# Kernel optimization log

Measured on AMD Instinct MI355X. Metric: run time of the kernel, lower is better.

Reference implementation:

```python
import jax, jax.numpy as jnp
import numpy as np

N_NODES = 24
BATCH = 65536

def _build_edge_index():
    # hard-coded 24-node supply-chain DAG from the source: node i (i<22, even pair)
    # connects to nodes 2*(i//2)+2 and 2*(i//2)+3
    rows, cols = [], []
    for i in range(22):
        base = 2 * (i // 2) + 2
        rows += [i, i]
        cols += [base, base + 1]
    return jnp.asarray(np.stack([rows, cols]), dtype=jnp.int64)  # [2, 44]


def setup_inputs() -> dict:
    key = jax.random.key(0)
    ks = jax.random.split(key, 4)
    x = jax.random.normal(ks[0], (BATCH, N_NODES, 10), dtype=jnp.float32)
    W1 = jax.random.normal(ks[1], (10, 64), dtype=jnp.float32) * (1.0 / np.sqrt(10))
    b1 = jnp.zeros((64,), dtype=jnp.float32)
    W3 = jax.random.normal(ks[2], (64, 64), dtype=jnp.float32) * (1.0 / 8.0)
    b3 = jnp.zeros((64,), dtype=jnp.float32)
    W2 = jax.random.normal(ks[3], (64, 10), dtype=jnp.float32) * (1.0 / 8.0)
    b2 = jnp.zeros((10,), dtype=jnp.float32)
    edge_index = _build_edge_index()
    return {"x": x, "W1": W1, "b1": b1, "W3": W3, "b3": b3,
            "W2": W2, "b2": b2, "edge_index": edge_index}


def _gcn_norm(edge_index, n_nodes):
    # PyG gcn_norm with add_self_loops=True: deg counted at target (col) index
    src, dst = edge_index[0], edge_index[1]
    deg = jnp.ones((n_nodes,), jnp.float32).at[dst].add(1.0)  # self loop contributes 1
    dinv = jax.lax.rsqrt(deg)
    norm_e = dinv[src] * dinv[dst]        # [E] edge weights
    norm_self = dinv * dinv               # [N] self-loop weights
    return src, dst, norm_e, norm_self


def _gcn_conv(h, W, b, src, dst, norm_e, norm_self):
    # h: [B, N, Fin] -> [B, N, Fout]
    hw = h @ W                                             # [B, N, Fout]
    msg = hw[:, src, :] * norm_e[None, :, None]            # gather + scale [B, E, Fout]
    agg = jnp.zeros_like(hw).at[:, dst, :].add(msg)        # scatter-add over targets
    agg = agg + hw * norm_self[None, :, None]              # self loops
    return agg + b


def reference(x, W1, b1, W3, b3, W2, b2, edge_index):
    src, dst, norm_e, norm_self = _gcn_norm(edge_index, x.shape[1])
    h = jax.nn.relu(_gcn_conv(x, W1, b1, src, dst, norm_e, norm_self))
    h = jax.nn.relu(_gcn_conv(h, W3, b3, src, dst, norm_e, norm_self))
    msg = jax.nn.relu(_gcn_conv(h, W2, b2, src, dst, norm_e, norm_self))  # [B, N, 10]
    pool = jnp.mean(msg, axis=1)  # global_mean_pool over the 24 nodes -> [B, 10]
    return pool
```

## Files before the change

### kernel.cpp

```cpp
#include <hip/hip_runtime.h>
#include <hip/hip_bf16.h>


typedef __attribute__((ext_vector_type(8))) short bf16x8;
typedef __attribute__((ext_vector_type(4))) float f32x4;

#define NBLK  1024
#define ITERS 8

__device__ __forceinline__ unsigned short f2bf(float f) {
  __hip_bfloat16 h = __float2bfloat16(f);
  return __builtin_bit_cast(unsigned short, h);
}
__device__ __forceinline__ float bflo(unsigned d) {
  return __builtin_bit_cast(float, d << 16);
}
__device__ __forceinline__ float bfhi(unsigned d) {
  return __builtin_bit_cast(float, d & 0xffff0000u);
}

union U16 { uint4 u; bf16x8 b; };

__device__ __forceinline__ bf16x8 pack8(const float v[8]) {
  U16 un;
  un.u.x = (unsigned)f2bf(v[0]) | ((unsigned)f2bf(v[1]) << 16);
  un.u.y = (unsigned)f2bf(v[2]) | ((unsigned)f2bf(v[3]) << 16);
  un.u.z = (unsigned)f2bf(v[4]) | ((unsigned)f2bf(v[5]) << 16);
  un.u.w = (unsigned)f2bf(v[6]) | ((unsigned)f2bf(v[7]) << 16);
  return un.b;
}

__global__ __launch_bounds__(256, 2)
void gnn_kernel(const float* __restrict__ xg,  const float* __restrict__ w1g,
                const float* __restrict__ b1g, const float* __restrict__ w3g,
                const float* __restrict__ b3g, const float* __restrict__ w2g,
                const float* __restrict__ b2g, float* __restrict__ outg) {
  __shared__ unsigned short hbuf_s[4][48 * 72];
  __shared__ float          o3_s[4][48 * 20];

  const int tid  = threadIdx.x;
  const int w    = tid >> 6;
  const int lane = tid & 63;
  const int l15  = lane & 15;
  const int g    = lane >> 4;
  unsigned short* hb = hbuf_s[w];
  float*          o3 = o3_s[w];
  const int wgid = blockIdx.x * 4 + w;

  bf16x8 w1f[4], w3f[4][2], w2f[2];
  {
    float v[8];
    #pragma unroll
    for (int mi = 0; mi < 4; ++mi) {
      const int c = 16 * mi + l15;
      #pragma unroll
      for (int j = 0; j < 8; ++j) { int k = 8 * g + j; v[j] = (k < 10) ? w1g[k * 64 + c] : 0.f; }
      w1f[mi] = pack8(v);
      #pragma unroll
      for (int ki = 0; ki < 2; ++ki) {
        #pragma unroll
        for (int j = 0; j < 8; ++j) { int k = 32 * ki + 8 * g + j; v[j] = w3g[k * 64 + c]; }
        w3f[mi][ki] = pack8(v);
      }
    }
    #pragma unroll
    for (int ki = 0; ki < 2; ++ki) {
      #pragma unroll
      for (int j = 0; j < 8; ++j) {
        int k = 32 * ki + 8 * g + j;
        v[j] = (l15 < 10) ? w2g[k * 10 + l15] : 0.f;
      }
      w2f[ki] = pack8(v);
    }
  }

  float b1r[2][8], b3r[2][8];
  #pragma unroll
  for (int ki = 0; ki < 2; ++ki) {
    float4 t0 = *(const float4*)&b1g[32 * ki + 8 * g];
    float4 t1 = *(const float4*)&b1g[32 * ki + 8 * g + 4];
    b1r[ki][0] = t0.x; b1r[ki][1] = t0.y; b1r[ki][2] = t0.z; b1r[ki][3] = t0.w;
    b1r[ki][4] = t1.x; b1r[ki][5] = t1.y; b1r[ki][6] = t1.z; b1r[ki][7] = t1.w;
    float4 s0v = *(const float4*)&b3g[32 * ki + 8 * g];
    float4 s1v = *(const float4*)&b3g[32 * ki + 8 * g + 4];
    b3r[ki][0] = s0v.x; b3r[ki][1] = s0v.y; b3r[ki][2] = s0v.z; b3r[ki][3] = s0v.w;
    b3r[ki][4] = s1v.x; b3r[ki][5] = s1v.y; b3r[ki][6] = s1v.z; b3r[ki][7] = s1v.w;
  }
  const float b2p = b2g[lane % 10];

  int rowA[3], rowB[3], xoff[3];
  float csv[3], cabv[3];
  #pragma unroll
  for (int ni = 0; ni < 3; ++ni) {
    const int r   = 16 * ni + l15;
    const int sub = r / 24;
    const int n   = r - 24 * sub;
    csv[ni]  = (n < 2) ? 1.f : (1.f / 3.f);
    cabv[ni] = (n < 2) ? 0.f : ((n < 4) ? 0.57735026918962576f : (1.f / 3.f));
    const int sA = (n < 4) ? 0 : ((n & ~1) - 2);
    const int sB = (n < 4) ? 1 : ((n & ~1) - 1);
    rowA[ni] = 24 * sub + sA;
    rowB[ni] = 24 * sub + sB;
    xoff[ni] = sub * 240 + n * 10;
  }

  auto build = [&](int ni, int ki, const float(&bias)[8]) -> bf16x8 {
    const int kbase = 32 * ki + 8 * g;
    const int rS = 16 * ni + l15;
    const uint4 vS = *(const uint4*)(hb + rS * 72 + kbase);
    const uint4 vA = *(const uint4*)(hb + rowA[ni] * 72 + kbase);
    const uint4 vB = *(const uint4*)(hb + rowB[ni] * 72 + kbase);
    const float cs = csv[ni], cab = cabv[ni];
    const unsigned aS[4] = {vS.x, vS.y, vS.z, vS.w};
    const unsigned aA[4] = {vA.x, vA.y, vA.z, vA.w};
    const unsigned aB[4] = {vB.x, vB.y, vB.z, vB.w};
    unsigned d[4];
    #pragma unroll
    for (int p = 0; p < 4; ++p) {
      float lo = fmaxf(cs * bflo(aS[p]) + cab * (bflo(aA[p]) + bflo(aB[p])) + bias[2 * p],     0.f);
      float hi = fmaxf(cs * bfhi(aS[p]) + cab * (bfhi(aA[p]) + bfhi(aB[p])) + bias[2 * p + 1], 0.f);
      d[p] = (unsigned)f2bf(lo) | ((unsigned)f2bf(hi) << 16);
    }
    U16 un; un.u.x = d[0]; un.u.y = d[1]; un.u.z = d[2]; un.u.w = d[3];
    return un.b;
  };

  const f32x4 zf = {0.f, 0.f, 0.f, 0.f};

  for (int it = 0; it < ITERS; ++it) {
    const int s0 = wgid * (2 * ITERS) + it * 2;
    const float* xb = xg + (long)s0 * 240;

    f32x4 acc[4][3];
    #pragma unroll
    for (int ni = 0; ni < 3; ++ni) {
      float v[8] = {0.f, 0.f, 0.f, 0.f, 0.f, 0.f, 0.f, 0.f};
      const float* xr = xb + xoff[ni];
      if (g == 0) {
        float2 p0 = *(const float2*)(xr + 0);
        float2 p1 = *(const float2*)(xr + 2);
        float2 p2 = *(const float2*)(xr + 4);
        float2 p3 = *(const float2*)(xr + 6);
        v[0] = p0.x; v[1] = p0.y; v[2] = p1.x; v[3] = p1.y;
        v[4] = p2.x; v[5] = p2.y; v[6] = p3.x; v[7] = p3.y;
      } else if (g == 1) {
        float2 p4 = *(const float2*)(xr + 8);
        v[0] = p4.x; v[1] = p4.y;
      }
      bf16x8 bx = pack8(v);
      #pragma unroll
      for (int mi = 0; mi < 4; ++mi)
        acc[mi][ni] = __builtin_amdgcn_mfma_f32_16x16x32_bf16(w1f[mi], bx, zf, 0, 0, 0);
    }
    #pragma unroll
    for (int mi = 0; mi < 4; ++mi) {
      #pragma unroll
      for (int ni = 0; ni < 3; ++ni) {
        const int r = 16 * ni + l15, cb = 16 * mi + 4 * g;
        uint2 pk;
        pk.x = (unsigned)f2bf(acc[mi][ni][0]) | ((unsigned)f2bf(acc[mi][ni][1]) << 16);
        pk.y = (unsigned)f2bf(acc[mi][ni][2]) | ((unsigned)f2bf(acc[mi][ni][3]) << 16);
        *(uint2*)(hb + r * 72 + cb) = pk;
      }
    }
    __syncthreads();

    #pragma unroll
    for (int ni = 0; ni < 3; ++ni) {
      bf16x8 bb0 = build(ni, 0, b1r[0]);
      bf16x8 bb1 = build(ni, 1, b1r[1]);
      #pragma unroll
      for (int mi = 0; mi < 4; ++mi) {
        f32x4 t = __builtin_amdgcn_mfma_f32_16x16x32_bf16(w3f[mi][0], bb0, zf, 0, 0, 0);
        acc[mi][ni] = __builtin_amdgcn_mfma_f32_16x16x32_bf16(w3f[mi][1], bb1, t, 0, 0, 0);
      }
    }
    #pragma unroll
    for (int mi = 0; mi < 4; ++mi) {
      #pragma unroll
      for (int ni = 0; ni < 3; ++ni) {
        const int r = 16 * ni + l15, cb = 16 * mi + 4 * g;
        uint2 pk;
        pk.x = (unsigned)f2bf(acc[mi][ni][0]) | ((unsigned)f2bf(acc[mi][ni][1]) << 16);
        pk.y = (unsigned)f2bf(acc[mi][ni][2]) | ((unsigned)f2bf(acc[mi][ni][3]) << 16);
        *(uint2*)(hb + r * 72 + cb) = pk;
      }
    }
    __syncthreads();

    f32x4 acc3[3];
    #pragma unroll
    for (int ni = 0; ni < 3; ++ni) {
      bf16x8 bb0 = build(ni, 0, b3r[0]);
      bf16x8 bb1 = build(ni, 1, b3r[1]);
      f32x4 t  = __builtin_amdgcn_mfma_f32_16x16x32_bf16(w2f[0], bb0, zf, 0, 0, 0);
      acc3[ni] = __builtin_amdgcn_mfma_f32_16x16x32_bf16(w2f[1], bb1, t, 0, 0, 0);
    }
    #pragma unroll
    for (int ni = 0; ni < 3; ++ni) {
      const int r = 16 * ni + l15;
      *(f32x4*)(o3 + r * 20 + 4 * g) = acc3[ni];
    }
    __syncthreads();

    {
      const int part = lane / 10;
      const int pc   = lane - 10 * part;
      #pragma unroll
      for (int sub = 0; sub < 2; ++sub) {
        float sum = 0.f;
        if (lane < 60) {
          const int rb = 24 * sub;
          #pragma unroll
          for (int dn = 0; dn < 4; ++dn) {
            const int n = 4 * part + dn;
            const float cs  = (n < 2) ? 1.f : (1.f / 3.f);
            const float cab = (n < 2) ? 0.f : ((n < 4) ? 0.57735026918962576f : (1.f / 3.f));
            const int sA = (n < 4) ? 0 : ((n & ~1) - 2);
            const int sB = (n < 4) ? 1 : ((n & ~1) - 1);
            const float vv = cs * o3[(rb + n) * 20 + pc]
                           + cab * (o3[(rb + sA) * 20 + pc] + o3[(rb + sB) * 20 + pc]);
            sum += fmaxf(vv + b2p, 0.f);
          }
        }
        float s1 = sum + __shfl_down(sum, 30);
        float t1 = __shfl_down(s1, 10);
        float t2 = __shfl_down(s1, 20);
        float tot = s1 + t1 + t2;
        if (lane < 10) outg[(long)(s0 + sub) * 10 + lane] = tot * (1.f / 24.f);
      }
    }
    __syncthreads();
  }
}

extern "C" void kernel_launch(void* const* d_in, const int* in_sizes, int n_in,
                              void* d_out, int out_size, void* d_ws, size_t ws_size,
                              hipStream_t stream) {
  (void)in_sizes; (void)n_in; (void)d_ws; (void)ws_size; (void)out_size;
  const float* x  = (const float*)d_in[0];
  const float* W1 = (const float*)d_in[1];
  const float* b1 = (const float*)d_in[2];
  const float* W3 = (const float*)d_in[3];
  const float* b3 = (const float*)d_in[4];
  const float* W2 = (const float*)d_in[5];
  const float* b2 = (const float*)d_in[6];
  float* out = (float*)d_out;
  hipLaunchKernelGGL(gnn_kernel, dim3(NBLK), dim3(256), 0, stream,
                     x, W1, b1, W3, b3, W2, b2, out);
}
```

Baseline: 209.7 us.

## Drop block barriers, alias LDS buffers, raise occupancy, use packed fp32 math

Removes every block-wide __syncthreads from the per-iteration loop. Each wave only touches its own private LDS slice, so in-wave LDS ordering is relied on instead of barriers. The layer-3 output buffer now shares storage with the hidden-state buffer, which cuts LDS per block, and launch bounds go from 2 to 4 blocks per CU. The aggregate-plus-ReLU step is rewritten with two-wide float vectors and elementwise fma/max so the compiler can emit packed fp32 instructions. The risk is that correctness now rests on wave-local LDS ordering and on the buffer aliasing, and the tighter register budget could cause spills.

```diff
diff --git a/kernel.cpp b/kernel.cpp
--- a/kernel.cpp
+++ b/kernel.cpp
@@ -4,6 +4,7 @@
 
 typedef __attribute__((ext_vector_type(8))) short bf16x8;
 typedef __attribute__((ext_vector_type(4))) float f32x4;
+typedef __attribute__((ext_vector_type(2))) float f32x2;
 
 #define NBLK  1024
 #define ITERS 8
@@ -12,11 +13,14 @@
   __hip_bfloat16 h = __float2bfloat16(f);
   return __builtin_bit_cast(unsigned short, h);
 }
-__device__ __forceinline__ float bflo(unsigned d) {
-  return __builtin_bit_cast(float, d << 16);
-}
-__device__ __forceinline__ float bfhi(unsigned d) {
-  return __builtin_bit_cast(float, d & 0xffff0000u);
+__device__ __forceinline__ f32x2 unpk(unsigned d) {
+  f32x2 r;
+  r.x = __builtin_bit_cast(float, d << 16);
+  r.y = __builtin_bit_cast(float, d & 0xffff0000u);
+  return r;
+}
+__device__ __forceinline__ unsigned pack2(f32x2 v) {
+  return (unsigned)f2bf(v.x) | ((unsigned)f2bf(v.y) << 16);
 }
 
 union U16 { uint4 u; bf16x8 b; };
@@ -30,13 +34,12 @@
   return un.b;
 }
 
-__global__ __launch_bounds__(256, 2)
+__global__ __launch_bounds__(256, 4)
 void gnn_kernel(const float* __restrict__ xg,  const float* __restrict__ w1g,
                 const float* __restrict__ b1g, const float* __restrict__ w3g,
                 const float* __restrict__ b3g, const float* __restrict__ w2g,
                 const float* __restrict__ b2g, float* __restrict__ outg) {
-  __shared__ unsigned short hbuf_s[4][48 * 72];
-  __shared__ float          o3_s[4][48 * 20];
+  __shared__ __align__(16) unsigned short hbuf_s[4][48 * 72];
 
   const int tid  = threadIdx.x;
   const int w    = tid >> 6;
@@ -44,7 +47,7 @@
   const int l15  = lane & 15;
   const int g    = lane >> 4;
   unsigned short* hb = hbuf_s[w];
-  float*          o3 = o3_s[w];
+  float*          o3 = (float*)hbuf_s[w];
   const int wgid = blockIdx.x * 4 + w;
 
   bf16x8 w1f[4], w3f[4][2], w2f[2];
@@ -74,17 +77,15 @@
     }
   }
 
-  float b1r[2][8], b3r[2][8];
+  f32x2 b1r[2][4], b3r[2][4];
   #pragma unroll
   for (int ki = 0; ki < 2; ++ki) {
-    float4 t0 = *(const float4*)&b1g[32 * ki + 8 * g];
-    float4 t1 = *(const float4*)&b1g[32 * ki + 8 * g + 4];
-    b1r[ki][0] = t0.x; b1r[ki][1] = t0.y; b1r[ki][2] = t0.z; b1r[ki][3] = t0.w;
-    b1r[ki][4] = t1.x; b1r[ki][5] = t1.y; b1r[ki][6] = t1.z; b1r[ki][7] = t1.w;
-    float4 s0v = *(const float4*)&b3g[32 * ki + 8 * g];
-    float4 s1v = *(const float4*)&b3g[32 * ki + 8 * g + 4];
-    b3r[ki][0] = s0v.x; b3r[ki][1] = s0v.y; b3r[ki][2] = s0v.z; b3r[ki][3] = s0v.w;
-    b3r[ki][4] = s1v.x; b3r[ki][5] = s1v.y; b3r[ki][6] = s1v.z; b3r[ki][7] = s1v.w;
+    #pragma unroll
+    for (int p = 0; p < 4; ++p) {
+      const int k = 32 * ki + 8 * g + 2 * p;
+      b1r[ki][p].x = b1g[k]; b1r[ki][p].y = b1g[k + 1];
+      b3r[ki][p].x = b3g[k]; b3r[ki][p].y = b3g[k + 1];
+    }
   }
   const float b2p = b2g[lane % 10];
 
@@ -104,22 +105,27 @@
     xoff[ni] = sub * 240 + n * 10;
   }
 
-  auto build = [&](int ni, int ki, const float(&bias)[8]) -> bf16x8 {
+  const f32x2 zero2 = {0.f, 0.f};
+
+  auto build = [&](int ni, int ki, const f32x2(&bias)[4]) -> bf16x8 {
     const int kbase = 32 * ki + 8 * g;
-    const int rS = 16 * ni + l15;
-    const uint4 vS = *(const uint4*)(hb + rS * 72 + kbase);
+    const uint4 vS = *(const uint4*)(hb + (16 * ni + l15) * 72 + kbase);
     const uint4 vA = *(const uint4*)(hb + rowA[ni] * 72 + kbase);
     const uint4 vB = *(const uint4*)(hb + rowB[ni] * 72 + kbase);
-    const float cs = csv[ni], cab = cabv[ni];
+    const f32x2 cs2  = {csv[ni], csv[ni]};
+    const f32x2 cab2 = {cabv[ni], cabv[ni]};
     const unsigned aS[4] = {vS.x, vS.y, vS.z, vS.w};
     const unsigned aA[4] = {vA.x, vA.y, vA.z, vA.w};
     const unsigned aB[4] = {vB.x, vB.y, vB.z, vB.w};
     unsigned d[4];
     #pragma unroll
     for (int p = 0; p < 4; ++p) {
-      float lo = fmaxf(cs * bflo(aS[p]) + cab * (bflo(aA[p]) + bflo(aB[p])) + bias[2 * p],     0.f);
-      float hi = fmaxf(cs * bfhi(aS[p]) + cab * (bfhi(aA[p]) + bfhi(aB[p])) + bias[2 * p + 1], 0.f);
-      d[p] = (unsigned)f2bf(lo) | ((unsigned)f2bf(hi) << 16);
+      f32x2 S = unpk(aS[p]);
+      f32x2 t = unpk(aA[p]) + unpk(aB[p]);
+      f32x2 v = __builtin_elementwise_fma(S, cs2, bias[p]);
+      v = __builtin_elementwise_fma(t, cab2, v);
+      v = __builtin_elementwise_max(v, zero2);
+      d[p] = pack2(v);
     }
     U16 un; un.u.x = d[0]; un.u.y = d[1]; un.u.z = d[2]; un.u.w = d[3];
     return un.b;
@@ -163,7 +169,6 @@
         *(uint2*)(hb + r * 72 + cb) = pk;
       }
     }
-    __syncthreads();
 
     #pragma unroll
     for (int ni = 0; ni < 3; ++ni) {
@@ -186,7 +191,6 @@
         *(uint2*)(hb + r * 72 + cb) = pk;
       }
     }
-    __syncthreads();
 
     f32x4 acc3[3];
     #pragma unroll
@@ -201,7 +205,6 @@
       const int r = 16 * ni + l15;
       *(f32x4*)(o3 + r * 20 + 4 * g) = acc3[ni];
     }
-    __syncthreads();
 
     {
       const int part = lane / 10;
@@ -230,7 +233,6 @@
         if (lane < 10) outg[(long)(s0 + sub) * 10 + lane] = tot * (1.f / 24.f);
       }
     }
-    __syncthreads();
   }
 }
 
```

After: 315.7 us. 50.6% more time.
